# Optimization experiments

Measured on AMD Instinct MI355X. Metric: run time of the kernel, lower is better.

## Reference

```python
import jax, jax.numpy as jnp
import numpy as np

N = 100000   # nodes
E = 1600000  # edges (before self-loops)
F = 128      # num_features
H = 128      # hidden_dim
EPS = 1e-5   # BatchNorm eps


def setup_inputs() -> dict:
    key = jax.random.key(0)
    ks = jax.random.split(key, 8)
    x = jax.random.normal(ks[0], (N, F), dtype=jnp.float32)
    edge_index = jax.random.randint(ks[1], (2, E), 0, N, dtype=jnp.int64)

    def lin(k, din, dout):
        s = 1.0 / np.sqrt(din)
        kw, kb = jax.random.split(k)
        W = jax.random.uniform(kw, (din, dout), jnp.float32, -s, s)
        b = jax.random.uniform(kb, (dout,), jnp.float32, -s, s)
        return W, b

    W1, b1 = lin(ks[2], F, H)
    W2, b2 = lin(ks[3], H, H)
    W3, b3 = lin(ks[4], H, H)
    Wc, bc = lin(ks[5], H, 2)

    def bn_params():
        return (jnp.ones((H,), jnp.float32), jnp.zeros((H,), jnp.float32),
                jnp.zeros((H,), jnp.float32), jnp.ones((H,), jnp.float32))

    g1, be1, rm1, rv1 = bn_params()
    g2, be2, rm2, rv2 = bn_params()
    g3, be3, rm3, rv3 = bn_params()

    return {"x": x, "edge_index": edge_index,
            "W1": W1, "b1": b1, "W2": W2, "b2": b2, "W3": W3, "b3": b3,
            "g1": g1, "be1": be1, "rm1": rm1, "rv1": rv1,
            "g2": g2, "be2": be2, "rm2": rm2, "rv2": rv2,
            "g3": g3, "be3": be3, "rm3": rm3, "rv3": rv3,
            "Wc": Wc, "bc": bc}


def _gcn_norm(edge_index, num_nodes):
    # add self-loops, compute symmetric normalization (PyG GCNConv default)
    loop = jnp.arange(num_nodes, dtype=edge_index.dtype)
    src = jnp.concatenate([edge_index[0], loop])
    dst = jnp.concatenate([edge_index[1], loop])
    deg = jax.ops.segment_sum(jnp.ones_like(dst, dtype=jnp.float32), dst,
                              num_segments=num_nodes)
    dinv = jnp.where(deg > 0, jax.lax.rsqrt(deg), 0.0)
    norm = dinv[src] * dinv[dst]  # [E+N]
    return src, dst, norm


def _gcn_conv(x, W, b, src, dst, norm, num_nodes):
    h = x @ W                              # [N, H] linear first
    msg = h[src] * norm[:, None]           # gather + scale  [E+N, H]
    out = jax.ops.segment_sum(msg, dst, num_segments=num_nodes)  # scatter-add
    return out + b


def _bn_eval(x, g, be, rm, rv):
    return (x - rm) * jax.lax.rsqrt(rv + EPS) * g + be


def reference(x, edge_index,
              W1, b1, W2, b2, W3, b3,
              g1, be1, rm1, rv1,
              g2, be2, rm2, rv2,
              g3, be3, rm3, rv3,
              Wc, bc):
    n = x.shape[0]
    src, dst, norm = _gcn_norm(edge_index, n)
    h = _gcn_conv(x, W1, b1, src, dst, norm, n)
    h = _bn_eval(jax.nn.relu(h), g1, be1, rm1, rv1)
    # dropout: identity in eval mode
    h = _gcn_conv(h, W2, b2, src, dst, norm, n)
    h = _bn_eval(jax.nn.relu(h), g2, be2, rm2, rv2)
    h = _gcn_conv(h, W3, b3, src, dst, norm, n)
    h = _bn_eval(jax.nn.relu(h), g3, be3, rm3, rv3)
    return h @ Wc + bc  # [N, 2]
```

## Files before the change

### kernel.cpp

```cpp
#include <hip/hip_runtime.h>
#include <hip/hip_fp16.h>

#define BN_EPS 1e-5f
#define CHUNK 4096
#define BBITS 7

typedef _Float16 half8 __attribute__((ext_vector_type(8)));
typedef float f32x4 __attribute__((ext_vector_type(4)));

__device__ __forceinline__ float4 f4zero() { return make_float4(0.f, 0.f, 0.f, 0.f); }


__global__ __launch_bounds__(256) void k_pack_hist(const float* __restrict__ W1,
                                                   const float* __restrict__ W2,
                                                   const float* __restrict__ W3,
                                                   _Float16* __restrict__ pW,
                                                   const int* __restrict__ dst,
                                                   int* __restrict__ tableT,
                                                   int nA, int nbuck, int e) {
    __shared__ int h[1024];
    int tid = threadIdx.x;
    if (blockIdx.x < 24) {
        int t = blockIdx.x * 256 + tid;
        int wi = t >> 11;
        int tt = t & 2047;
        const float* W = (wi == 0) ? W1 : ((wi == 1) ? W2 : W3);
        int kc = tt >> 9;
        int rem = tt & 511;
        int ct = rem >> 6;
        int lane = rem & 63;
        int q = lane >> 4;
        int col = ct * 16 + (lane & 15);
        half8 hh;
#pragma unroll
        for (int j = 0; j < 8; ++j)
            hh[j] = (_Float16)W[(kc * 32 + q * 8 + j) * 128 + col];
        *(half8*)(pW + (size_t)t * 8) = hh;
        return;
    }
    int blk = blockIdx.x - 24;
    for (int k = tid; k < 1024; k += 256) h[k] = 0;
    __syncthreads();
    int base = blk * CHUNK;
    if (base + CHUNK <= e && (e & 3) == 0) {
        const int4* d4 = (const int4*)(dst + base);
#pragma unroll
        for (int t = 0; t < CHUNK / 1024; ++t) {
            int4 d = d4[t * 256 + tid];
            atomicAdd(&h[d.x >> BBITS], 1);
            atomicAdd(&h[d.y >> BBITS], 1);
            atomicAdd(&h[d.z >> BBITS], 1);
            atomicAdd(&h[d.w >> BBITS], 1);
        }
    } else {
        for (int i = base + tid; i < e && i < base + CHUNK; i += 256)
            atomicAdd(&h[dst[i] >> BBITS], 1);
    }
    __syncthreads();
    for (int k = tid; k < nbuck; k += 256)
        tableT[(size_t)k * nA + blk] = h[k];
}


__global__ __launch_bounds__(1024) void k_scan_block(const int* __restrict__ in,
                                                     int* __restrict__ outp,
                                                     int* __restrict__ partials, int len) {
    __shared__ int s[1024];
    int t = threadIdx.x;
    int gid = blockIdx.x * 1024 + t;
    int v = (gid < len) ? in[gid] : 0;
    int x = v;
    s[t] = x;
    __syncthreads();
    for (int d = 1; d < 1024; d <<= 1) {
        int y = (t >= d) ? s[t - d] : 0;
        __syncthreads();
        x += y;
        s[t] = x;
        __syncthreads();
    }
    if (gid < len) outp[gid] = x - v;
    if (t == 1023) partials[blockIdx.x] = x;
}

__global__ __launch_bounds__(256) void k_scan_addp(int* __restrict__ data,
                                                   const int* __restrict__ partials, int len) {
    __shared__ int red[256];
    int tid = threadIdx.x;
    int K = blockIdx.x >> 2;
    int s = 0;
    for (int t = tid; t < K; t += 256) s += partials[t];
    red[tid] = s;
    __syncthreads();
    for (int d = 128; d > 0; d >>= 1) {
        if (tid < d) red[tid] += red[tid + d];
        __syncthreads();
    }
    int gid = blockIdx.x * 256 + tid;
    if (gid < len) data[gid] += red[0];
}


__global__ __launch_bounds__(256) void k_bucket_scatter(const int* __restrict__ src,
                                                        const int* __restrict__ dst,
                                                        const int* __restrict__ tableT,
                                                        int2* __restrict__ bed,
                                                        int nA, int nbuck, int e) {
    __shared__ int cur[1024];
    int blk = blockIdx.x, tid = threadIdx.x;
    for (int k = tid; k < nbuck; k += 256)
        cur[k] = tableT[(size_t)k * nA + blk];
    __syncthreads();
    int base = blk * CHUNK;
    if (base + CHUNK <= e && (e & 3) == 0) {
        const int4* s4 = (const int4*)(src + base);
        const int4* d4 = (const int4*)(dst + base);
#pragma unroll
        for (int t = 0; t < CHUNK / 1024; ++t) {
            int4 s = s4[t * 256 + tid];
            int4 d = d4[t * 256 + tid];
            int p0 = atomicAdd(&cur[d.x >> BBITS], 1); bed[p0] = make_int2(s.x, d.x);
            int p1 = atomicAdd(&cur[d.y >> BBITS], 1); bed[p1] = make_int2(s.y, d.y);
            int p2 = atomicAdd(&cur[d.z >> BBITS], 1); bed[p2] = make_int2(s.z, d.z);
            int p3 = atomicAdd(&cur[d.w >> BBITS], 1); bed[p3] = make_int2(s.w, d.w);
        }
    } else {
        for (int i = base + tid; i < e && i < base + CHUNK; i += 256) {
            int d = dst[i];
            int p = atomicAdd(&cur[d >> BBITS], 1);
            bed[p] = make_int2(src[i], d);
        }
    }
}


__global__ __launch_bounds__(256) void k_bucket_rank(const int2* __restrict__ bed,
                                                     const int* __restrict__ tableT,
                                                     int* __restrict__ brank,
                                                     int* __restrict__ counts,
                                                     float* __restrict__ dinv,
                                                     int* __restrict__ localOff,
                                                     int* __restrict__ btot,
                                                     int nA, int nbuck, int n, int e) {
    __shared__ int lcnt[128];
    __shared__ int lscan[128];
    int b = blockIdx.x, tid = threadIdx.x;
    if (tid < 128) lcnt[tid] = 0;
    __syncthreads();
    int start = tableT[(size_t)b * nA];
    int end = (b + 1 < nbuck) ? tableT[(size_t)(b + 1) * nA] : e;
    for (int i = start + tid; i < end; i += 256) {
        int2 q = bed[i];
        brank[i] = atomicAdd(&lcnt[q.y & 127], 1);
    }
    __syncthreads();
    int padded = 0;
    if (tid < 128) {
        padded = (lcnt[tid] + 7) & ~7;
        lscan[tid] = padded;
    }
    __syncthreads();
    for (int d = 1; d < 128; d <<= 1) {
        int y = (tid < 128 && tid >= d) ? lscan[tid - d] : 0;
        __syncthreads();
        if (tid < 128) lscan[tid] += y;
        __syncthreads();
    }
    if (tid < 128) {
        int node = (b << BBITS) + tid;
        if (node < n) {
            int c = lcnt[tid];
            counts[node] = c;
            dinv[node] = rsqrtf((float)(c + 1));
            localOff[node] = lscan[tid] - padded;
        }
        if (tid == 127) btot[b] = lscan[127];
    }
}


__global__ __launch_bounds__(1024) void k_scan_buckets(const int* __restrict__ btot,
                                                       int* __restrict__ bucketBase, int nbuck) {
    __shared__ int s[1024];
    int t = threadIdx.x;
    int v = (t < nbuck) ? btot[t] : 0;
    int x = v;
    s[t] = x;
    __syncthreads();
    for (int d = 1; d < 1024; d <<= 1) {
        int y = (t >= d) ? s[t - d] : 0;
        __syncthreads();
        x += y;
        s[t] = x;
        __syncthreads();
    }
    if (t < nbuck) bucketBase[t] = x - v;
    if (t == nbuck - 1) bucketBase[nbuck] = x;
}


__global__ __launch_bounds__(256) void k_finalize(const int* __restrict__ counts,
                                                  const int* __restrict__ localOff,
                                                  const int* __restrict__ bucketBase,
                                                  int* __restrict__ offs,
                                                  int* __restrict__ er,
                                                  const int2* __restrict__ bed,
                                                  const int* __restrict__ brank,
                                                  unsigned int* __restrict__ bufAzero,
                                                  int n, int e, int gN, int nbuck) {
    int tid = threadIdx.x;
    if (blockIdx.x < gN) {
        int node = blockIdx.x * 256 + tid;
        if (node < n) {
            int c = counts[node];
            int o = bucketBase[node >> BBITS] + localOff[node];
            offs[node] = o;
            int pc = (c + 7) & ~7;
            for (int j = c; j < pc; ++j) er[o + j] = n << 8;
        }
        if (node == 0) offs[n] = bucketBase[nbuck];
        if (blockIdx.x == 0 && tid < 64) bufAzero[tid] = 0u;
    } else {
        int i = ((blockIdx.x - gN) * 256 + tid) * 2;
        if (i + 1 < e) {
            int4 q = *(const int4*)(bed + i);
            int2 r = *(const int2*)(brank + i);
            er[bucketBase[q.y >> BBITS] + localOff[q.y] + r.x] = q.x << 8;
            er[bucketBase[q.w >> BBITS] + localOff[q.w] + r.y] = q.z << 8;
        } else if (i < e) {
            int2 q = bed[i];
            er[bucketBase[q.y >> BBITS] + localOff[q.y] + brank[i]] = q.x << 8;
        }
    }
}


template <bool AF32>
__global__ __launch_bounds__(256) void k_gemm_mfma(const void* __restrict__ Av,
                                                   const _Float16* __restrict__ pW,
                                                   const float* __restrict__ dinv,
                                                   uint4* __restrict__ C, int n) {
    __shared__ char smem[32768];
    uint4* sW = (uint4*)smem;
    int tid = threadIdx.x;

    {
        const uint4* gW = (const uint4*)pW;
#pragma unroll
        for (int i = 0; i < 8; ++i) sW[tid + 256 * i] = gW[tid + 256 * i];
    }
    __syncthreads();

    int wave = tid >> 6, lane = tid & 63;
    int quad = lane >> 4, l16 = lane & 15;
    int row0 = blockIdx.x * 64 + wave * 16;
    int arow = row0 + l16;
    int arowc = (arow < n) ? arow : (n - 1);

    half8 af[4];
    if (AF32) {
        const float* A = (const float*)Av + (size_t)arowc * 128 + quad * 8;
#pragma unroll
        for (int kc = 0; kc < 4; ++kc) {
            float4 lo = *(const float4*)(A + kc * 32);
            float4 hi = *(const float4*)(A + kc * 32 + 4);
            half8 h;
            h[0] = (_Float16)lo.x; h[1] = (_Float16)lo.y;
            h[2] = (_Float16)lo.z; h[3] = (_Float16)lo.w;
            h[4] = (_Float16)hi.x; h[5] = (_Float16)hi.y;
            h[6] = (_Float16)hi.z; h[7] = (_Float16)hi.w;
            af[kc] = h;
        }
    } else {
        const _Float16* A = (const _Float16*)Av + (size_t)arowc * 128 + quad * 8;
#pragma unroll
        for (int kc = 0; kc < 4; ++kc)
            af[kc] = *(const half8*)(A + kc * 32);
    }

    f32x4 acc[8];
#pragma unroll
    for (int ct = 0; ct < 8; ++ct) acc[ct] = (f32x4){0.f, 0.f, 0.f, 0.f};

#pragma unroll
    for (int kc = 0; kc < 4; ++kc) {
#pragma unroll
        for (int ct = 0; ct < 8; ++ct) {
            half8 bf = *(half8*)&sW[(kc * 8 + ct) * 64 + lane];
            acc[ct] = __builtin_amdgcn_mfma_f32_16x16x32_f16(af[kc], bf, acc[ct], 0, 0, 0);
        }
    }

    __syncthreads();

    _Float16* eb = (_Float16*)smem + wave * 16 * 136;
    float dv[4];
#pragma unroll
    for (int r = 0; r < 4; ++r) {
        int rr = row0 + quad * 4 + r;
        dv[r] = dinv[(rr < n) ? rr : (n - 1)];
    }
#pragma unroll
    for (int ct = 0; ct < 8; ++ct)
#pragma unroll
        for (int r = 0; r < 4; ++r)
            eb[(quad * 4 + r) * 136 + ct * 16 + l16] = (_Float16)(acc[ct][r] * dv[r]);

#pragma unroll
    for (int i = 0; i < 4; ++i) {
        int linear = i * 64 + lane;
        int r = linear >> 4, c = linear & 15;
        uint4 v = *(uint4*)((char*)eb + r * 272 + c * 16);
        int row = row0 + r;
        if (row < n) C[(size_t)row * 16 + c] = v;
    }
}


__device__ __forceinline__ void acc_row(float4& acc, uint2 q) {
    asm("v_fma_mix_f32 %0, %1, 1.0, %0 op_sel:[0,0,0] op_sel_hi:[1,0,0]" : "+v"(acc.x) : "v"(q.x));
    asm("v_fma_mix_f32 %0, %1, 1.0, %0 op_sel:[1,0,0] op_sel_hi:[1,0,0]" : "+v"(acc.y) : "v"(q.x));
    asm("v_fma_mix_f32 %0, %1, 1.0, %0 op_sel:[0,0,0] op_sel_hi:[1,0,0]" : "+v"(acc.z) : "v"(q.y));
    asm("v_fma_mix_f32 %0, %1, 1.0, %0 op_sel:[1,0,0] op_sel_hi:[1,0,0]" : "+v"(acc.w) : "v"(q.y));
}

template <bool FUSE_CLS>
__global__ __launch_bounds__(256) void k_aggregate(const uint2* __restrict__ Ah,
                                                   const int* __restrict__ offs,
                                                   const int* __restrict__ er,
                                                   const float* __restrict__ dinv,
                                                   const float* __restrict__ bias,
                                                   const float* __restrict__ g,
                                                   const float* __restrict__ be,
                                                   const float* __restrict__ rm,
                                                   const float* __restrict__ rv,
                                                   uint2* __restrict__ Hout,
                                                   const float* __restrict__ Wc,
                                                   const float* __restrict__ bc,
                                                   float* __restrict__ out, int n) {
    int lane = threadIdx.x & 31;
    int node = blockIdx.x * 8 + (threadIdx.x >> 5);
    if (node >= n) return;

    const char* AhB = (const char*)Ah;
    unsigned int l8 = (unsigned int)lane * 8u;

    float4 acc = f4zero();
    acc_row(acc, *(const uint2*)(AhB + (((unsigned int)node << 8) + l8)));

    int e0 = offs[node], e1 = offs[node + 1];
    for (int e = e0; e < e1; e += 8) {
        int4 ra = *(const int4*)(er + e);
        int4 rb = *(const int4*)(er + e + 4);
        uint2 v0 = *(const uint2*)(AhB + ((unsigned int)ra.x + l8));
        uint2 v1 = *(const uint2*)(AhB + ((unsigned int)ra.y + l8));
        uint2 v2 = *(const uint2*)(AhB + ((unsigned int)ra.z + l8));
        uint2 v3 = *(const uint2*)(AhB + ((unsigned int)ra.w + l8));
        uint2 v4 = *(const uint2*)(AhB + ((unsigned int)rb.x + l8));
        uint2 v5 = *(const uint2*)(AhB + ((unsigned int)rb.y + l8));
        uint2 v6 = *(const uint2*)(AhB + ((unsigned int)rb.z + l8));
        uint2 v7 = *(const uint2*)(AhB + ((unsigned int)rb.w + l8));
        acc_row(acc, v0); acc_row(acc, v1); acc_row(acc, v2); acc_row(acc, v3);
        acc_row(acc, v4); acc_row(acc, v5); acc_row(acc, v6); acc_row(acc, v7);
    }

    float di = dinv[node];
    acc.x *= di; acc.y *= di; acc.z *= di; acc.w *= di;

    float4 b4  = ((const float4*)bias)[lane];
    float4 g4  = ((const float4*)g)[lane];
    float4 be4 = ((const float4*)be)[lane];
    float4 rm4 = ((const float4*)rm)[lane];
    float4 rv4 = ((const float4*)rv)[lane];

    float4 o;
    float v;
    v = fmaxf(acc.x + b4.x, 0.f); o.x = (v - rm4.x) * rsqrtf(rv4.x + BN_EPS) * g4.x + be4.x;
    v = fmaxf(acc.y + b4.y, 0.f); o.y = (v - rm4.y) * rsqrtf(rv4.y + BN_EPS) * g4.y + be4.y;
    v = fmaxf(acc.z + b4.z, 0.f); o.z = (v - rm4.z) * rsqrtf(rv4.z + BN_EPS) * g4.z + be4.z;
    v = fmaxf(acc.w + b4.w, 0.f); o.w = (v - rm4.w) * rsqrtf(rv4.w + BN_EPS) * g4.w + be4.w;

    if (!FUSE_CLS) {
        __half2 p0 = __floats2half2_rn(o.x, o.y);
        __half2 p1 = __floats2half2_rn(o.z, o.w);
        uint2 u;
        u.x = *(unsigned int*)&p0;
        u.y = *(unsigned int*)&p1;
        Hout[(size_t)node * 32 + lane] = u;
    } else {
        const float4* Wv = (const float4*)Wc;
        float4 w01 = Wv[2 * lane];
        float4 w23 = Wv[2 * lane + 1];
        float p0 = o.x * w01.x + o.y * w01.z + o.z * w23.x + o.w * w23.z;
        float p1 = o.x * w01.y + o.y * w01.w + o.z * w23.y + o.w * w23.w;
#pragma unroll
        for (int d = 16; d >= 1; d >>= 1) {
            p0 += __shfl_down(p0, d, 32);
            p1 += __shfl_down(p1, d, 32);
        }
        if (lane == 0) {
            out[node * 2 + 0] = p0 + bc[0];
            out[node * 2 + 1] = p1 + bc[1];
        }
    }
}


extern "C" void kernel_launch(void* const* d_in, const int* in_sizes, int n_in,
                              void* d_out, int out_size, void* d_ws, size_t ws_size,
                              hipStream_t stream) {
    const float* x   = (const float*)d_in[0];
    const int*   ei  = (const int*)d_in[1];
    const float* W1  = (const float*)d_in[2];
    const float* b1  = (const float*)d_in[3];
    const float* W2  = (const float*)d_in[4];
    const float* b2  = (const float*)d_in[5];
    const float* W3  = (const float*)d_in[6];
    const float* b3  = (const float*)d_in[7];
    const float* g1  = (const float*)d_in[8];
    const float* be1 = (const float*)d_in[9];
    const float* rm1 = (const float*)d_in[10];
    const float* rv1 = (const float*)d_in[11];
    const float* g2  = (const float*)d_in[12];
    const float* be2 = (const float*)d_in[13];
    const float* rm2 = (const float*)d_in[14];
    const float* rv2 = (const float*)d_in[15];
    const float* g3  = (const float*)d_in[16];
    const float* be3 = (const float*)d_in[17];
    const float* rm3 = (const float*)d_in[18];
    const float* rv3 = (const float*)d_in[19];
    const float* Wc  = (const float*)d_in[20];
    const float* bc  = (const float*)d_in[21];
    float* out = (float*)d_out;

    int n = in_sizes[0] / 128;
    int e = in_sizes[1] / 2;
    const int* src = ei;
    const int* dst = ei + e;

    char* ws = (char*)d_ws;
    size_t off = 0;
    auto alloc = [&](size_t bytes) -> char* {
        char* p = ws + off;
        off += (bytes + 255) & ~(size_t)255;
        return p;
    };
    int nA    = (e + CHUNK - 1) / CHUNK;
    int nbuck = (n + (1 << BBITS) - 1) >> BBITS;
    int tlen  = nbuck * nA;
    int erCap = e + 8 * n;

    char*      bufA     = (char*) alloc((size_t)(n + 1) * 256);
    char*      bufH     = (char*) alloc((size_t)n * 256);
    float*     dinv     = (float*)alloc((size_t)n * 4);
    int*       counts   = (int*)  alloc((size_t)n * 4);
    int*       offs     = (int*)  alloc((size_t)(n + 1) * 4);
    int*       localOff = (int*)  alloc((size_t)n * 4);
    int*       btot     = (int*)  alloc((size_t)(nbuck + 1) * 4);
    int*       bktBase  = (int*)  alloc((size_t)(nbuck + 1) * 4);
    int*       tableT   = (int*)  alloc((size_t)(tlen + 1) * 4);
    int*       parts    = (int*)  alloc(8192);
    int*       er       = (int*)  alloc((size_t)erCap * 4);
    _Float16*  pW       = (_Float16*)alloc(3 * 16384 * 2);
    (void)ws_size; (void)n_in; (void)out_size;

    int2* bed   = (int2*)bufH;
    int*  brank = (int*)(bufH + (size_t)e * 8);

    int gN  = (n + 255) / 256;
    int nbT = (tlen + 1023) / 1024;

    k_pack_hist<<<24 + nA, 256, 0, stream>>>(W1, W2, W3, pW, dst, tableT, nA, nbuck, e);
    k_scan_block<<<nbT, 1024, 0, stream>>>(tableT, tableT, parts, tlen);
    k_scan_addp<<<(tlen + 255) / 256, 256, 0, stream>>>(tableT, parts, tlen);
    k_bucket_scatter<<<nA, 256, 0, stream>>>(src, dst, tableT, bed, nA, nbuck, e);
    k_bucket_rank<<<nbuck, 256, 0, stream>>>(bed, tableT, brank, counts, dinv, localOff,
                                             btot, nA, nbuck, n, e);
    k_scan_buckets<<<1, 1024, 0, stream>>>(btot, bktBase, nbuck);
    int gP = gN + (e / 2 + 255) / 256 + 1;
    k_finalize<<<gP, 256, 0, stream>>>(counts, localOff, bktBase, offs, er, bed, brank,
                                       (unsigned int*)(bufA + (size_t)n * 256), n, e, gN, nbuck);

    int gGemm = (n + 63) / 64;
    int gAgg  = (n + 7) / 8;

    k_gemm_mfma<true><<<gGemm, 256, 0, stream>>>(x, pW, dinv, (uint4*)bufA, n);
    k_aggregate<false><<<gAgg, 256, 0, stream>>>((const uint2*)bufA, offs, er, dinv,
                                                 b1, g1, be1, rm1, rv1, (uint2*)bufH,
                                                 nullptr, nullptr, nullptr, n);

    k_gemm_mfma<false><<<gGemm, 256, 0, stream>>>(bufH, pW + 16384, dinv, (uint4*)bufA, n);
    k_aggregate<false><<<gAgg, 256, 0, stream>>>((const uint2*)bufA, offs, er, dinv,
                                                 b2, g2, be2, rm2, rv2, (uint2*)bufH,
                                                 nullptr, nullptr, nullptr, n);

    k_gemm_mfma<false><<<gGemm, 256, 0, stream>>>(bufH, pW + 32768, dinv, (uint4*)bufA, n);
    k_aggregate<true><<<gAgg, 256, 0, stream>>>((const uint2*)bufA, offs, er, dinv,
                                                b3, g3, be3, rm3, rv3, nullptr,
                                                Wc, bc, out, n);
}
```

Measured before the change: 395.4 us.

## Fuse aggregation with next-layer GEMM and merge finalize with first GEMM

Each aggregation kernel for layers 1 and 2 now keeps the post-ReLU/BN fp16 rows of a 64-node tile in shared memory and runs the next layer's MFMA GEMM directly on them. This removes the intermediate H write/read and two kernel launches. The CSR finalize pass and the first-layer GEMM are merged into one launch using a block-index split. The cost is that each block now processes 8 nodes per 32-lane group sequentially before the GEMM, which adds imbalance and latency from uneven degrees. It also reads GEMM weights from global memory instead of LDS.

Result: no change. 398.9 us (+0.9%).

```diff
diff --git a/kernel.cpp b/kernel.cpp
--- a/kernel.cpp
+++ b/kernel.cpp
@@ -199,51 +199,13 @@
 }
 
 
-__global__ __launch_bounds__(256) void k_finalize(const int* __restrict__ counts,
-                                                  const int* __restrict__ localOff,
-                                                  const int* __restrict__ bucketBase,
-                                                  int* __restrict__ offs,
-                                                  int* __restrict__ er,
-                                                  const int2* __restrict__ bed,
-                                                  const int* __restrict__ brank,
-                                                  unsigned int* __restrict__ bufAzero,
-                                                  int n, int e, int gN, int nbuck) {
-    int tid = threadIdx.x;
-    if (blockIdx.x < gN) {
-        int node = blockIdx.x * 256 + tid;
-        if (node < n) {
-            int c = counts[node];
-            int o = bucketBase[node >> BBITS] + localOff[node];
-            offs[node] = o;
-            int pc = (c + 7) & ~7;
-            for (int j = c; j < pc; ++j) er[o + j] = n << 8;
-        }
-        if (node == 0) offs[n] = bucketBase[nbuck];
-        if (blockIdx.x == 0 && tid < 64) bufAzero[tid] = 0u;
-    } else {
-        int i = ((blockIdx.x - gN) * 256 + tid) * 2;
-        if (i + 1 < e) {
-            int4 q = *(const int4*)(bed + i);
-            int2 r = *(const int2*)(brank + i);
-            er[bucketBase[q.y >> BBITS] + localOff[q.y] + r.x] = q.x << 8;
-            er[bucketBase[q.w >> BBITS] + localOff[q.w] + r.y] = q.z << 8;
-        } else if (i < e) {
-            int2 q = bed[i];
-            er[bucketBase[q.y >> BBITS] + localOff[q.y] + brank[i]] = q.x << 8;
-        }
-    }
-}
-
-
 template <bool AF32>
-__global__ __launch_bounds__(256) void k_gemm_mfma(const void* __restrict__ Av,
-                                                   const _Float16* __restrict__ pW,
-                                                   const float* __restrict__ dinv,
-                                                   uint4* __restrict__ C, int n) {
-    __shared__ char smem[32768];
+__device__ __forceinline__ void gemm_body(int bid, int tid, char* smem,
+                                          const void* __restrict__ Av,
+                                          const _Float16* __restrict__ pW,
+                                          const float* __restrict__ dinv,
+                                          uint4* __restrict__ C, int n) {
     uint4* sW = (uint4*)smem;
-    int tid = threadIdx.x;
-
     {
         const uint4* gW = (const uint4*)pW;
 #pragma unroll
@@ -253,7 +215,7 @@
 
     int wave = tid >> 6, lane = tid & 63;
     int quad = lane >> 4, l16 = lane & 15;
-    int row0 = blockIdx.x * 64 + wave * 16;
+    int row0 = bid * 64 + wave * 16;
     int arow = row0 + l16;
     int arowc = (arow < n) ? arow : (n - 1);
 
@@ -317,6 +279,54 @@
 }
 
 
+__global__ __launch_bounds__(256) void k_finalize_gemm(const int* __restrict__ counts,
+                                                       const int* __restrict__ localOff,
+                                                       const int* __restrict__ bucketBase,
+                                                       int* __restrict__ offs,
+                                                       int* __restrict__ er,
+                                                       const int2* __restrict__ bed,
+                                                       const int* __restrict__ brank,
+                                                       unsigned int* __restrict__ bufAzero,
+                                                       unsigned int* __restrict__ bufHzero,
+                                                       const float* __restrict__ x,
+                                                       const _Float16* __restrict__ pW,
+                                                       const float* __restrict__ dinv,
+                                                       uint4* __restrict__ C,
+                                                       int n, int e, int gN, int nbuck, int gFin) {
+    __shared__ char smem[32768];
+    int tid = threadIdx.x;
+    int bid = blockIdx.x;
+    if (bid >= gFin) {
+        gemm_body<true>(bid - gFin, tid, smem, x, pW, dinv, C, n);
+        return;
+    }
+    if (bid < gN) {
+        int node = bid * 256 + tid;
+        if (node < n) {
+            int c = counts[node];
+            int o = bucketBase[node >> BBITS] + localOff[node];
+            offs[node] = o;
+            int pc = (c + 7) & ~7;
+            for (int j = c; j < pc; ++j) er[o + j] = n << 8;
+        }
+        if (node == 0) offs[n] = bucketBase[nbuck];
+        if (bid == 0 && tid < 64) bufAzero[tid] = 0u;
+        if (bid == 1 && tid < 64) bufHzero[tid] = 0u;
+    } else {
+        int i = ((bid - gN) * 256 + tid) * 2;
+        if (i + 1 < e) {
+            int4 q = *(const int4*)(bed + i);
+            int2 r = *(const int2*)(brank + i);
+            er[bucketBase[q.y >> BBITS] + localOff[q.y] + r.x] = q.x << 8;
+            er[bucketBase[q.w >> BBITS] + localOff[q.w] + r.y] = q.z << 8;
+        } else if (i < e) {
+            int2 q = bed[i];
+            er[bucketBase[q.y >> BBITS] + localOff[q.y] + brank[i]] = q.x << 8;
+        }
+    }
+}
+
+
 __device__ __forceinline__ void acc_row(float4& acc, uint2 q) {
     asm("v_fma_mix_f32 %0, %1, 1.0, %0 op_sel:[0,0,0] op_sel_hi:[1,0,0]" : "+v"(acc.x) : "v"(q.x));
     asm("v_fma_mix_f32 %0, %1, 1.0, %0 op_sel:[1,0,0] op_sel_hi:[1,0,0]" : "+v"(acc.y) : "v"(q.x));
@@ -324,20 +334,137 @@
     asm("v_fma_mix_f32 %0, %1, 1.0, %0 op_sel:[1,0,0] op_sel_hi:[1,0,0]" : "+v"(acc.w) : "v"(q.y));
 }
 
-template <bool FUSE_CLS>
-__global__ __launch_bounds__(256) void k_aggregate(const uint2* __restrict__ Ah,
-                                                   const int* __restrict__ offs,
-                                                   const int* __restrict__ er,
-                                                   const float* __restrict__ dinv,
-                                                   const float* __restrict__ bias,
-                                                   const float* __restrict__ g,
-                                                   const float* __restrict__ be,
-                                                   const float* __restrict__ rm,
-                                                   const float* __restrict__ rv,
-                                                   uint2* __restrict__ Hout,
-                                                   const float* __restrict__ Wc,
-                                                   const float* __restrict__ bc,
-                                                   float* __restrict__ out, int n) {
+
+__global__ __launch_bounds__(256) void k_agg_gemm(const uint2* __restrict__ Ah,
+                                                  const int* __restrict__ offs,
+                                                  const int* __restrict__ er,
+                                                  const float* __restrict__ dinv,
+                                                  const float* __restrict__ bias,
+                                                  const float* __restrict__ g,
+                                                  const float* __restrict__ be,
+                                                  const float* __restrict__ rm,
+                                                  const float* __restrict__ rv,
+                                                  const _Float16* __restrict__ pW,
+                                                  uint4* __restrict__ C, int n) {
+    __shared__ _Float16 sA[64 * 136];
+    int tid = threadIdx.x;
+    int lane32 = tid & 31, grp = tid >> 5;
+    int nbase = blockIdx.x * 64;
+    const char* AhB = (const char*)Ah;
+    unsigned int l8 = (unsigned int)lane32 * 8u;
+
+    float4 b4  = ((const float4*)bias)[lane32];
+    float4 g4  = ((const float4*)g)[lane32];
+    float4 be4 = ((const float4*)be)[lane32];
+    float4 rm4 = ((const float4*)rm)[lane32];
+    float4 rv4 = ((const float4*)rv)[lane32];
+    float4 sc;
+    sc.x = rsqrtf(rv4.x + BN_EPS) * g4.x;
+    sc.y = rsqrtf(rv4.y + BN_EPS) * g4.y;
+    sc.z = rsqrtf(rv4.z + BN_EPS) * g4.z;
+    sc.w = rsqrtf(rv4.w + BN_EPS) * g4.w;
+
+    for (int j = 0; j < 8; ++j) {
+        int row = grp * 8 + j;
+        int node = nbase + row;
+        if (node >= n) break;
+
+        float4 acc = f4zero();
+        acc_row(acc, *(const uint2*)(AhB + (((unsigned int)node << 8) + l8)));
+
+        int e0 = offs[node], e1 = offs[node + 1];
+        for (int e = e0; e < e1; e += 8) {
+            int4 ra = *(const int4*)(er + e);
+            int4 rb = *(const int4*)(er + e + 4);
+            uint2 v0 = *(const uint2*)(AhB + ((unsigned int)ra.x + l8));
+            uint2 v1 = *(const uint2*)(AhB + ((unsigned int)ra.y + l8));
+            uint2 v2 = *(const uint2*)(AhB + ((unsigned int)ra.z + l8));
+            uint2 v3 = *(const uint2*)(AhB + ((unsigned int)ra.w + l8));
+            uint2 v4 = *(const uint2*)(AhB + ((unsigned int)rb.x + l8));
+            uint2 v5 = *(const uint2*)(AhB + ((unsigned int)rb.y + l8));
+            uint2 v6 = *(const uint2*)(AhB + ((unsigned int)rb.z + l8));
+            uint2 v7 = *(const uint2*)(AhB + ((unsigned int)rb.w + l8));
+            acc_row(acc, v0); acc_row(acc, v1); acc_row(acc, v2); acc_row(acc, v3);
+            acc_row(acc, v4); acc_row(acc, v5); acc_row(acc, v6); acc_row(acc, v7);
+        }
+
+        float di = dinv[node];
+        float4 o;
+        float v;
+        v = fmaxf(acc.x * di + b4.x, 0.f); o.x = (v - rm4.x) * sc.x + be4.x;
+        v = fmaxf(acc.y * di + b4.y, 0.f); o.y = (v - rm4.y) * sc.y + be4.y;
+        v = fmaxf(acc.z * di + b4.z, 0.f); o.z = (v - rm4.z) * sc.z + be4.z;
+        v = fmaxf(acc.w * di + b4.w, 0.f); o.w = (v - rm4.w) * sc.w + be4.w;
+
+        __half2 p0 = __floats2half2_rn(o.x, o.y);
+        __half2 p1 = __floats2half2_rn(o.z, o.w);
+        uint2 u;
+        u.x = *(unsigned int*)&p0;
+        u.y = *(unsigned int*)&p1;
+        *(uint2*)&sA[row * 136 + lane32 * 4] = u;
+    }
+    __syncthreads();
+
+    int wave = tid >> 6, lane = tid & 63;
+    int quad = lane >> 4, l16 = lane & 15;
+    int row0 = wave * 16;
+
+    half8 af[4];
+#pragma unroll
+    for (int kc = 0; kc < 4; ++kc)
+        af[kc] = *(const half8*)&sA[(row0 + l16) * 136 + kc * 32 + quad * 8];
+
+    f32x4 acc[8];
+#pragma unroll
+    for (int ct = 0; ct < 8; ++ct) acc[ct] = (f32x4){0.f, 0.f, 0.f, 0.f};
+
+#pragma unroll
+    for (int kc = 0; kc < 4; ++kc) {
+#pragma unroll
+        for (int ct = 0; ct < 8; ++ct) {
+            half8 bf = *(const half8*)(pW + (size_t)((kc * 8 + ct) * 64 + lane) * 8);
+            acc[ct] = __builtin_amdgcn_mfma_f32_16x16x32_f16(af[kc], bf, acc[ct], 0, 0, 0);
+        }
+    }
+
+    __syncthreads();
+
+    _Float16* eb = sA + wave * 16 * 136;
+    float dv[4];
+#pragma unroll
+    for (int r = 0; r < 4; ++r) {
+        int rr = nbase + row0 + quad * 4 + r;
+        dv[r] = dinv[(rr < n) ? rr : (n - 1)];
+    }
+#pragma unroll
+    for (int ct = 0; ct < 8; ++ct)
+#pragma unroll
+        for (int r = 0; r < 4; ++r)
+            eb[(quad * 4 + r) * 136 + ct * 16 + l16] = (_Float16)(acc[ct][r] * dv[r]);
+
+#pragma unroll
+    for (int i = 0; i < 4; ++i) {
+        int linear = i * 64 + lane;
+        int r = linear >> 4, c = linear & 15;
+        uint4 v = *(uint4*)((char*)eb + r * 272 + c * 16);
+        int row = nbase + row0 + r;
+        if (row < n) C[(size_t)row * 16 + c] = v;
+    }
+}
+
+
+__global__ __launch_bounds__(256) void k_aggregate_cls(const uint2* __restrict__ Ah,
+                                                       const int* __restrict__ offs,
+                                                       const int* __restrict__ er,
+                                                       const float* __restrict__ dinv,
+                                                       const float* __restrict__ bias,
+                                                       const float* __restrict__ g,
+                                                       const float* __restrict__ be,
+                                                       const float* __restrict__ rm,
+                                                       const float* __restrict__ rv,
+                                                       const float* __restrict__ Wc,
+                                                       const float* __restrict__ bc,
+                                                       float* __restrict__ out, int n) {
     int lane = threadIdx.x & 31;
     int node = blockIdx.x * 8 + (threadIdx.x >> 5);
     if (node >= n) return;
@@ -380,28 +507,19 @@
     v = fmaxf(acc.z + b4.z, 0.f); o.z = (v - rm4.z) * rsqrtf(rv4.z + BN_EPS) * g4.z + be4.z;
     v = fmaxf(acc.w + b4.w, 0.f); o.w = (v - rm4.w) * rsqrtf(rv4.w + BN_EPS) * g4.w + be4.w;
 
-    if (!FUSE_CLS) {
-        __half2 p0 = __floats2half2_rn(o.x, o.y);
-        __half2 p1 = __floats2half2_rn(o.z, o.w);
-        uint2 u;
-        u.x = *(unsigned int*)&p0;
-        u.y = *(unsigned int*)&p1;
-        Hout[(size_t)node * 32 + lane] = u;
-    } else {
-        const float4* Wv = (const float4*)Wc;
-        float4 w01 = Wv[2 * lane];
-        float4 w23 = Wv[2 * lane + 1];
-        float p0 = o.x * w01.x + o.y * w01.z + o.z * w23.x + o.w * w23.z;
-        float p1 = o.x * w01.y + o.y * w01.w + o.z * w23.y + o.w * w23.w;
-#pragma unroll
-        for (int d = 16; d >= 1; d >>= 1) {
-            p0 += __shfl_down(p0, d, 32);
-            p1 += __shfl_down(p1, d, 32);
-        }
-        if (lane == 0) {
-            out[node * 2 + 0] = p0 + bc[0];
-            out[node * 2 + 1] = p1 + bc[1];
-        }
+    const float4* Wv = (const float4*)Wc;
+    float4 w01 = Wv[2 * lane];
+    float4 w23 = Wv[2 * lane + 1];
+    float p0 = o.x * w01.x + o.y * w01.z + o.z * w23.x + o.w * w23.z;
+    float p1 = o.x * w01.y + o.y * w01.w + o.z * w23.y + o.w * w23.w;
+#pragma unroll
+    for (int d = 16; d >= 1; d >>= 1) {
+        p0 += __shfl_down(p0, d, 32);
+        p1 += __shfl_down(p1, d, 32);
+    }
+    if (lane == 0) {
+        out[node * 2 + 0] = p0 + bc[0];
+        out[node * 2 + 1] = p1 + bc[1];
     }
 }
 
@@ -451,7 +569,7 @@
     int erCap = e + 8 * n;
 
     char*      bufA     = (char*) alloc((size_t)(n + 1) * 256);
-    char*      bufH     = (char*) alloc((size_t)n * 256);
+    char*      bufH     = (char*) alloc((size_t)(n + 1) * 256);
     float*     dinv     = (float*)alloc((size_t)n * 4);
     int*       counts   = (int*)  alloc((size_t)n * 4);
     int*       offs     = (int*)  alloc((size_t)(n + 1) * 4);
@@ -477,25 +595,24 @@
     k_bucket_rank<<<nbuck, 256, 0, stream>>>(bed, tableT, brank, counts, dinv, localOff,
                                              btot, nA, nbuck, n, e);
     k_scan_buckets<<<1, 1024, 0, stream>>>(btot, bktBase, nbuck);
-    int gP = gN + (e / 2 + 255) / 256 + 1;
-    k_finalize<<<gP, 256, 0, stream>>>(counts, localOff, bktBase, offs, er, bed, brank,
-                                       (unsigned int*)(bufA + (size_t)n * 256), n, e, gN, nbuck);
 
     int gGemm = (n + 63) / 64;
+    int gFin  = gN + (e / 2 + 255) / 256 + 1;
+    k_finalize_gemm<<<gFin + gGemm, 256, 0, stream>>>(
+        counts, localOff, bktBase, offs, er, bed, brank,
+        (unsigned int*)(bufA + (size_t)n * 256),
+        (unsigned int*)(bufH + (size_t)n * 256),
+        x, pW, dinv, (uint4*)bufA, n, e, gN, nbuck, gFin);
+
+    int gAggF = (n + 63) / 64;
     int gAgg  = (n + 7) / 8;
 
-    k_gemm_mfma<true><<<gGemm, 256, 0, stream>>>(x, pW, dinv, (uint4*)bufA, n);
-    k_aggregate<false><<<gAgg, 256, 0, stream>>>((const uint2*)bufA, offs, er, dinv,
-                                                 b1, g1, be1, rm1, rv1, (uint2*)bufH,
-                                                 nullptr, nullptr, nullptr, n);
-
-    k_gemm_mfma<false><<<gGemm, 256, 0, stream>>>(bufH, pW + 16384, dinv, (uint4*)bufA, n);
-    k_aggregate<false><<<gAgg, 256, 0, stream>>>((const uint2*)bufA, offs, er, dinv,
-                                                 b2, g2, be2, rm2, rv2, (uint2*)bufH,
-                                                 nullptr, nullptr, nullptr, n);
-
-    k_gemm_mfma<false><<<gGemm, 256, 0, stream>>>(bufH, pW + 32768, dinv, (uint4*)bufA, n);
-    k_aggregate<true><<<gAgg, 256, 0, stream>>>((const uint2*)bufA, offs, er, dinv,
-                                                b3, g3, be3, rm3, rv3, nullptr,
-                                                Wc, bc, out, n);
-}
+    k_agg_gemm<<<gAggF, 256, 0, stream>>>((const uint2*)bufA, offs, er, dinv,
+                                          b1, g1, be1, rm1, rv1,
+                                          pW + 16384, (uint4*)bufH, n);
+    k_agg_gemm<<<gAggF, 256, 0, stream>>>((const uint2*)bufH, offs, er, dinv,
+                                          b2, g2, be2, rm2, rv2,
+                                          pW + 32768, (uint4*)bufA, n);
+    k_aggregate_cls<<<gAgg, 256, 0, stream>>>((const uint2*)bufA, offs, er, dinv,
+                                              b3, g3, be3, rm3, rv3, Wc, bc, out, n);
+}
```

## Replace bucketed CSR build with global-atomic counting sort fused with first GEMM

Applied to the files above, without the earlier changes.

Drops the two-level bucket histogram, scatter, rank and finalize pipeline and builds the CSR with per-node global atomic counts, a single padded scan that also computes dinv, and a cursor-based atomic placement pass. The placement and padding work is fused into one launch alongside the first-layer GEMM blocks, which cuts several kernel launches and the intermediate bed/brank buffers. In exchange, edge order within each node becomes nondeterministic, which can change float summation order. It also relies on heavy global atomic contention on the count and cursor arrays.

Measured after the change: 500.0 us. 1.26x slower.

```diff
diff --git a/kernel.cpp b/kernel.cpp
--- a/kernel.cpp
+++ b/kernel.cpp
@@ -3,12 +3,17 @@
 
 #define BN_EPS 1e-5f
 #define CHUNK 4096
-#define BBITS 7
 
 typedef _Float16 half8 __attribute__((ext_vector_type(8)));
 typedef float f32x4 __attribute__((ext_vector_type(4)));
 
 __device__ __forceinline__ float4 f4zero() { return make_float4(0.f, 0.f, 0.f, 0.f); }
+
+
+__global__ __launch_bounds__(256) void k_zero(int4* __restrict__ p, int len4) {
+    int i = blockIdx.x * 256 + threadIdx.x;
+    if (i < len4) p[i] = make_int4(0, 0, 0, 0);
+}
 
 
 __global__ __launch_bounds__(256) void k_pack_hist(const float* __restrict__ W1,
@@ -16,9 +21,7 @@
                                                    const float* __restrict__ W3,
                                                    _Float16* __restrict__ pW,
                                                    const int* __restrict__ dst,
-                                                   int* __restrict__ tableT,
-                                                   int nA, int nbuck, int e) {
-    __shared__ int h[1024];
+                                                   int* __restrict__ counts, int e) {
     int tid = threadIdx.x;
     if (blockIdx.x < 24) {
         int t = blockIdx.x * 256 + tid;
@@ -38,37 +41,34 @@
         *(half8*)(pW + (size_t)t * 8) = hh;
         return;
     }
-    int blk = blockIdx.x - 24;
-    for (int k = tid; k < 1024; k += 256) h[k] = 0;
-    __syncthreads();
-    int base = blk * CHUNK;
-    if (base + CHUNK <= e && (e & 3) == 0) {
+    int base = (blockIdx.x - 24) * CHUNK;
+    if (base + CHUNK <= e) {
         const int4* d4 = (const int4*)(dst + base);
 #pragma unroll
         for (int t = 0; t < CHUNK / 1024; ++t) {
             int4 d = d4[t * 256 + tid];
-            atomicAdd(&h[d.x >> BBITS], 1);
-            atomicAdd(&h[d.y >> BBITS], 1);
-            atomicAdd(&h[d.z >> BBITS], 1);
-            atomicAdd(&h[d.w >> BBITS], 1);
+            atomicAdd(&counts[d.x], 1);
+            atomicAdd(&counts[d.y], 1);
+            atomicAdd(&counts[d.z], 1);
+            atomicAdd(&counts[d.w], 1);
         }
     } else {
-        for (int i = base + tid; i < e && i < base + CHUNK; i += 256)
-            atomicAdd(&h[dst[i] >> BBITS], 1);
-    }
-    __syncthreads();
-    for (int k = tid; k < nbuck; k += 256)
-        tableT[(size_t)k * nA + blk] = h[k];
-}
-
-
-__global__ __launch_bounds__(1024) void k_scan_block(const int* __restrict__ in,
-                                                     int* __restrict__ outp,
-                                                     int* __restrict__ partials, int len) {
+        for (int i = base + tid; i < e; i += 256)
+            atomicAdd(&counts[dst[i]], 1);
+    }
+}
+
+
+__global__ __launch_bounds__(1024) void k_scan_dinv(const int* __restrict__ counts,
+                                                    int* __restrict__ offs,
+                                                    float* __restrict__ dinv,
+                                                    int* __restrict__ partials, int n) {
     __shared__ int s[1024];
     int t = threadIdx.x;
     int gid = blockIdx.x * 1024 + t;
-    int v = (gid < len) ? in[gid] : 0;
+    int c = (gid < n) ? counts[gid] : 0;
+    if (gid < n) dinv[gid] = rsqrtf((float)(c + 1));
+    int v = (c + 7) & ~7;
     int x = v;
     s[t] = x;
     __syncthreads();
@@ -79,7 +79,7 @@
         s[t] = x;
         __syncthreads();
     }
-    if (gid < len) outp[gid] = x - v;
+    if (gid < n) offs[gid] = x - v;
     if (t == 1023) partials[blockIdx.x] = x;
 }
 
@@ -101,149 +101,13 @@
 }
 
 
-__global__ __launch_bounds__(256) void k_bucket_scatter(const int* __restrict__ src,
-                                                        const int* __restrict__ dst,
-                                                        const int* __restrict__ tableT,
-                                                        int2* __restrict__ bed,
-                                                        int nA, int nbuck, int e) {
-    __shared__ int cur[1024];
-    int blk = blockIdx.x, tid = threadIdx.x;
-    for (int k = tid; k < nbuck; k += 256)
-        cur[k] = tableT[(size_t)k * nA + blk];
-    __syncthreads();
-    int base = blk * CHUNK;
-    if (base + CHUNK <= e && (e & 3) == 0) {
-        const int4* s4 = (const int4*)(src + base);
-        const int4* d4 = (const int4*)(dst + base);
-#pragma unroll
-        for (int t = 0; t < CHUNK / 1024; ++t) {
-            int4 s = s4[t * 256 + tid];
-            int4 d = d4[t * 256 + tid];
-            int p0 = atomicAdd(&cur[d.x >> BBITS], 1); bed[p0] = make_int2(s.x, d.x);
-            int p1 = atomicAdd(&cur[d.y >> BBITS], 1); bed[p1] = make_int2(s.y, d.y);
-            int p2 = atomicAdd(&cur[d.z >> BBITS], 1); bed[p2] = make_int2(s.z, d.z);
-            int p3 = atomicAdd(&cur[d.w >> BBITS], 1); bed[p3] = make_int2(s.w, d.w);
-        }
-    } else {
-        for (int i = base + tid; i < e && i < base + CHUNK; i += 256) {
-            int d = dst[i];
-            int p = atomicAdd(&cur[d >> BBITS], 1);
-            bed[p] = make_int2(src[i], d);
-        }
-    }
-}
-
-
-__global__ __launch_bounds__(256) void k_bucket_rank(const int2* __restrict__ bed,
-                                                     const int* __restrict__ tableT,
-                                                     int* __restrict__ brank,
-                                                     int* __restrict__ counts,
-                                                     float* __restrict__ dinv,
-                                                     int* __restrict__ localOff,
-                                                     int* __restrict__ btot,
-                                                     int nA, int nbuck, int n, int e) {
-    __shared__ int lcnt[128];
-    __shared__ int lscan[128];
-    int b = blockIdx.x, tid = threadIdx.x;
-    if (tid < 128) lcnt[tid] = 0;
-    __syncthreads();
-    int start = tableT[(size_t)b * nA];
-    int end = (b + 1 < nbuck) ? tableT[(size_t)(b + 1) * nA] : e;
-    for (int i = start + tid; i < end; i += 256) {
-        int2 q = bed[i];
-        brank[i] = atomicAdd(&lcnt[q.y & 127], 1);
-    }
-    __syncthreads();
-    int padded = 0;
-    if (tid < 128) {
-        padded = (lcnt[tid] + 7) & ~7;
-        lscan[tid] = padded;
-    }
-    __syncthreads();
-    for (int d = 1; d < 128; d <<= 1) {
-        int y = (tid < 128 && tid >= d) ? lscan[tid - d] : 0;
-        __syncthreads();
-        if (tid < 128) lscan[tid] += y;
-        __syncthreads();
-    }
-    if (tid < 128) {
-        int node = (b << BBITS) + tid;
-        if (node < n) {
-            int c = lcnt[tid];
-            counts[node] = c;
-            dinv[node] = rsqrtf((float)(c + 1));
-            localOff[node] = lscan[tid] - padded;
-        }
-        if (tid == 127) btot[b] = lscan[127];
-    }
-}
-
-
-__global__ __launch_bounds__(1024) void k_scan_buckets(const int* __restrict__ btot,
-                                                       int* __restrict__ bucketBase, int nbuck) {
-    __shared__ int s[1024];
-    int t = threadIdx.x;
-    int v = (t < nbuck) ? btot[t] : 0;
-    int x = v;
-    s[t] = x;
-    __syncthreads();
-    for (int d = 1; d < 1024; d <<= 1) {
-        int y = (t >= d) ? s[t - d] : 0;
-        __syncthreads();
-        x += y;
-        s[t] = x;
-        __syncthreads();
-    }
-    if (t < nbuck) bucketBase[t] = x - v;
-    if (t == nbuck - 1) bucketBase[nbuck] = x;
-}
-
-
-__global__ __launch_bounds__(256) void k_finalize(const int* __restrict__ counts,
-                                                  const int* __restrict__ localOff,
-                                                  const int* __restrict__ bucketBase,
-                                                  int* __restrict__ offs,
-                                                  int* __restrict__ er,
-                                                  const int2* __restrict__ bed,
-                                                  const int* __restrict__ brank,
-                                                  unsigned int* __restrict__ bufAzero,
-                                                  int n, int e, int gN, int nbuck) {
-    int tid = threadIdx.x;
-    if (blockIdx.x < gN) {
-        int node = blockIdx.x * 256 + tid;
-        if (node < n) {
-            int c = counts[node];
-            int o = bucketBase[node >> BBITS] + localOff[node];
-            offs[node] = o;
-            int pc = (c + 7) & ~7;
-            for (int j = c; j < pc; ++j) er[o + j] = n << 8;
-        }
-        if (node == 0) offs[n] = bucketBase[nbuck];
-        if (blockIdx.x == 0 && tid < 64) bufAzero[tid] = 0u;
-    } else {
-        int i = ((blockIdx.x - gN) * 256 + tid) * 2;
-        if (i + 1 < e) {
-            int4 q = *(const int4*)(bed + i);
-            int2 r = *(const int2*)(brank + i);
-            er[bucketBase[q.y >> BBITS] + localOff[q.y] + r.x] = q.x << 8;
-            er[bucketBase[q.w >> BBITS] + localOff[q.w] + r.y] = q.z << 8;
-        } else if (i < e) {
-            int2 q = bed[i];
-            er[bucketBase[q.y >> BBITS] + localOff[q.y] + brank[i]] = q.x << 8;
-        }
-    }
-}
-
-
 template <bool AF32>
-__global__ __launch_bounds__(256) void k_gemm_mfma(const void* __restrict__ Av,
-                                                   const _Float16* __restrict__ pW,
-                                                   const float* __restrict__ dinv,
-                                                   uint4* __restrict__ C, int n) {
-    __shared__ char smem[32768];
+__device__ __forceinline__ void gemm_body(int bid, int tid, char* smem,
+                                          const void* __restrict__ Av,
+                                          const _Float16* __restrict__ pW,
+                                          const float* __restrict__ dinv,
+                                          uint4* __restrict__ C, int n) {
     uint4* sW = (uint4*)smem;
-    int tid = threadIdx.x;
-
     {
         const uint4* gW = (const uint4*)pW;
 #pragma unroll
@@ -253,7 +117,7 @@
 
     int wave = tid >> 6, lane = tid & 63;
     int quad = lane >> 4, l16 = lane & 15;
-    int row0 = blockIdx.x * 64 + wave * 16;
+    int row0 = bid * 64 + wave * 16;
     int arow = row0 + l16;
     int arowc = (arow < n) ? arow : (n - 1);
 
@@ -316,6 +180,65 @@
     }
 }
 
+__global__ __launch_bounds__(256) void k_gemm_mfma(const void* __restrict__ Av,
+                                                   const _Float16* __restrict__ pW,
+                                                   const float* __restrict__ dinv,
+                                                   uint4* __restrict__ C, int n) {
+    __shared__ char smem[32768];
+    gemm_body<false>(blockIdx.x, threadIdx.x, smem, Av, pW, dinv, C, n);
+}
+
+
+__global__ __launch_bounds__(256) void k_place_gemm(const int* __restrict__ src,
+                                                    const int* __restrict__ dst,
+                                                    const int* __restrict__ counts,
+                                                    int* __restrict__ offs,
+                                                    int* __restrict__ cursor,
+                                                    int* __restrict__ er,
+                                                    unsigned int* __restrict__ bufAzero,
+                                                    unsigned int* __restrict__ bufHzero,
+                                                    const float* __restrict__ x,
+                                                    const _Float16* __restrict__ pW,
+                                                    const float* __restrict__ dinv,
+                                                    uint4* __restrict__ C,
+                                                    int n, int e, int gN, int nE) {
+    __shared__ char smem[32768];
+    int tid = threadIdx.x;
+    int bid = blockIdx.x;
+    if (bid >= gN + nE) {
+        gemm_body<true>(bid - gN - nE, tid, smem, x, pW, dinv, C, n);
+        return;
+    }
+    if (bid < gN) {
+        int node = bid * 256 + tid;
+        if (node < n) {
+            int c = counts[node];
+            int o = offs[node];
+            int pc = (c + 7) & ~7;
+            for (int j = c; j < pc; ++j) er[o + j] = n << 8;
+            if (node == n - 1) offs[n] = o + pc;
+        }
+        if (bid == 0 && tid < 64) bufAzero[tid] = 0u;
+        if (bid == 1 && tid < 64) bufHzero[tid] = 0u;
+    } else {
+        int base = (bid - gN) * 1024;
+        if (base + 1024 <= e) {
+            int4 s = ((const int4*)(src + base))[tid];
+            int4 d = ((const int4*)(dst + base))[tid];
+            int o0 = atomicAdd(&cursor[d.x], 1); er[offs[d.x] + o0] = s.x << 8;
+            int o1 = atomicAdd(&cursor[d.y], 1); er[offs[d.y] + o1] = s.y << 8;
+            int o2 = atomicAdd(&cursor[d.z], 1); er[offs[d.z] + o2] = s.z << 8;
+            int o3 = atomicAdd(&cursor[d.w], 1); er[offs[d.w] + o3] = s.w << 8;
+        } else {
+            for (int i = base + tid; i < e; i += 256) {
+                int dd = dst[i], ss = src[i];
+                int o = atomicAdd(&cursor[dd], 1);
+                er[offs[dd] + o] = ss << 8;
+            }
+        }
+    }
+}
+
 
 __device__ __forceinline__ void acc_row(float4& acc, uint2 q) {
     asm("v_fma_mix_f32 %0, %1, 1.0, %0 op_sel:[0,0,0] op_sel_hi:[1,0,0]" : "+v"(acc.x) : "v"(q.x));
@@ -323,6 +246,7 @@
     asm("v_fma_mix_f32 %0, %1, 1.0, %0 op_sel:[0,0,0] op_sel_hi:[1,0,0]" : "+v"(acc.z) : "v"(q.y));
     asm("v_fma_mix_f32 %0, %1, 1.0, %0 op_sel:[1,0,0] op_sel_hi:[1,0,0]" : "+v"(acc.w) : "v"(q.y));
 }
+
 
 template <bool FUSE_CLS>
 __global__ __launch_bounds__(256) void k_aggregate(const uint2* __restrict__ Ah,
@@ -445,56 +369,46 @@
         off += (bytes + 255) & ~(size_t)255;
         return p;
     };
-    int nA    = (e + CHUNK - 1) / CHUNK;
-    int nbuck = (n + (1 << BBITS) - 1) >> BBITS;
-    int tlen  = nbuck * nA;
     int erCap = e + 8 * n;
 
     char*      bufA     = (char*) alloc((size_t)(n + 1) * 256);
-    char*      bufH     = (char*) alloc((size_t)n * 256);
+    char*      bufH     = (char*) alloc((size_t)(n + 1) * 256);
     float*     dinv     = (float*)alloc((size_t)n * 4);
-    int*       counts   = (int*)  alloc((size_t)n * 4);
+    int*       cc       = (int*)  alloc((size_t)2 * n * 4);
     int*       offs     = (int*)  alloc((size_t)(n + 1) * 4);
-    int*       localOff = (int*)  alloc((size_t)n * 4);
-    int*       btot     = (int*)  alloc((size_t)(nbuck + 1) * 4);
-    int*       bktBase  = (int*)  alloc((size_t)(nbuck + 1) * 4);
-    int*       tableT   = (int*)  alloc((size_t)(tlen + 1) * 4);
     int*       parts    = (int*)  alloc(8192);
     int*       er       = (int*)  alloc((size_t)erCap * 4);
     _Float16*  pW       = (_Float16*)alloc(3 * 16384 * 2);
     (void)ws_size; (void)n_in; (void)out_size;
 
-    int2* bed   = (int2*)bufH;
-    int*  brank = (int*)(bufH + (size_t)e * 8);
-
-    int gN  = (n + 255) / 256;
-    int nbT = (tlen + 1023) / 1024;
-
-    k_pack_hist<<<24 + nA, 256, 0, stream>>>(W1, W2, W3, pW, dst, tableT, nA, nbuck, e);
-    k_scan_block<<<nbT, 1024, 0, stream>>>(tableT, tableT, parts, tlen);
-    k_scan_addp<<<(tlen + 255) / 256, 256, 0, stream>>>(tableT, parts, tlen);
-    k_bucket_scatter<<<nA, 256, 0, stream>>>(src, dst, tableT, bed, nA, nbuck, e);
-    k_bucket_rank<<<nbuck, 256, 0, stream>>>(bed, tableT, brank, counts, dinv, localOff,
-                                             btot, nA, nbuck, n, e);
-    k_scan_buckets<<<1, 1024, 0, stream>>>(btot, bktBase, nbuck);
-    int gP = gN + (e / 2 + 255) / 256 + 1;
-    k_finalize<<<gP, 256, 0, stream>>>(counts, localOff, bktBase, offs, er, bed, brank,
-                                       (unsigned int*)(bufA + (size_t)n * 256), n, e, gN, nbuck);
-
+    int* counts = cc;
+    int* cursor = cc + n;
+
+    int nA    = (e + CHUNK - 1) / CHUNK;
+    int gN    = (n + 255) / 256;
+    int nE    = (e + 1023) / 1024;
     int gGemm = (n + 63) / 64;
     int gAgg  = (n + 7) / 8;
-
-    k_gemm_mfma<true><<<gGemm, 256, 0, stream>>>(x, pW, dinv, (uint4*)bufA, n);
+    int len4  = (2 * n + 3) / 4;
+
+    k_zero<<<(len4 + 255) / 256, 256, 0, stream>>>((int4*)cc, len4);
+    k_pack_hist<<<24 + nA, 256, 0, stream>>>(W1, W2, W3, pW, dst, counts, e);
+    k_scan_dinv<<<(n + 1023) / 1024, 1024, 0, stream>>>(counts, offs, dinv, parts, n);
+    k_scan_addp<<<(n + 255) / 256, 256, 0, stream>>>(offs, parts, n);
+    k_place_gemm<<<gN + nE + gGemm, 256, 0, stream>>>(
+        src, dst, counts, offs, cursor, er,
+        (unsigned int*)(bufA + (size_t)n * 256),
+        (unsigned int*)(bufH + (size_t)n * 256),
+        x, pW, dinv, (uint4*)bufA, n, e, gN, nE);
+
     k_aggregate<false><<<gAgg, 256, 0, stream>>>((const uint2*)bufA, offs, er, dinv,
                                                  b1, g1, be1, rm1, rv1, (uint2*)bufH,
                                                  nullptr, nullptr, nullptr, n);
-
-    k_gemm_mfma<false><<<gGemm, 256, 0, stream>>>(bufH, pW + 16384, dinv, (uint4*)bufA, n);
+    k_gemm_mfma<<<gGemm, 256, 0, stream>>>(bufH, pW + 16384, dinv, (uint4*)bufA, n);
     k_aggregate<false><<<gAgg, 256, 0, stream>>>((const uint2*)bufA, offs, er, dinv,
                                                  b2, g2, be2, rm2, rv2, (uint2*)bufH,
                                                  nullptr, nullptr, nullptr, n);
-
-    k_gemm_mfma<false><<<gGemm, 256, 0, stream>>>(bufH, pW + 32768, dinv, (uint4*)bufA, n);
+    k_gemm_mfma<<<gGemm, 256, 0, stream>>>(bufH, pW + 32768, dinv, (uint4*)bufA, n);
     k_aggregate<true><<<gAgg, 256, 0, stream>>>((const uint2*)bufA, offs, er, dinv,
                                                 b3, g3, be3, rm3, rv3, nullptr,
                                                 Wc, bc, out, n);
```
